# Kernel optimization log

Hardware: AMD Instinct MI355X
Metric: run time of the kernel (lower is better)

The kernel has to match this reference:

```python
import jax, jax.numpy as jnp
import numpy as np

# irreps config: (multiplicity, l) for "128x0e + 64x1o + 32x2e" (in == out)
IRREPS = [(128, 0), (64, 1), (32, 2)]


def setup_inputs() -> dict:
    key = jax.random.key(0)
    k0, k1, k2, k3 = jax.random.split(key, 4)
    N = 200000
    dim = sum(mul * (2 * l + 1) for mul, l in IRREPS)  # 480
    x = jax.random.normal(k0, (N, dim), dtype=jnp.float32)
    W0 = jax.random.normal(k1, (128, 128), dtype=jnp.float32)
    W1 = jax.random.normal(k2, (64, 64), dtype=jnp.float32)
    W2 = jax.random.normal(k3, (32, 32), dtype=jnp.float32)
    return {"x": x, "W0": W0, "W1": W1, "W2": W2}


def _irrep_linear(x, weights):
    # x: [N, dim_in]; per-irrep: reshape block to [N, mul, 2l+1], contract mul dim,
    # scale by 1/sqrt(fan_in) = 1/sqrt(mul_in) (e3nn default path normalization).
    outs = []
    off = 0
    for (mul, l), W in zip(IRREPS, weights):
        d = 2 * l + 1
        blk = x[:, off:off + mul * d].reshape(-1, mul, d)  # [N, mul, d]
        alpha = 1.0 / np.sqrt(mul)
        y = jnp.einsum('nid,io->nod', blk, W) * jnp.float32(alpha)  # [N, mul_out, d]
        outs.append(y.reshape(-1, mul * d))
        off += mul * d
    return jnp.concatenate(outs, axis=-1)  # [N, dim_out]


def reference(x, W0, W1, W2):
    return _irrep_linear(x, (W0, W1, W2))
```

## Files before the change

kernel.cpp:

```cpp
#include <hip/hip_runtime.h>

typedef _Float16 v8h __attribute__((ext_vector_type(8)));
typedef float    v4f __attribute__((ext_vector_type(4)));

#define MFMA16(a, b, c) __builtin_amdgcn_mfma_f32_16x16x32_f16((a), (b), (c), 0, 0, 0)

#define GLL16(gptr, lptr)                                                        \
  __builtin_amdgcn_global_load_lds((const __attribute__((address_space(1))) void*)(gptr), \
                                   (__attribute__((address_space(3))) void*)(lptr), 16, 0, 0)


__global__ void build_frags_k(const float* __restrict__ W0, const float* __restrict__ W1,
                              const float* __restrict__ W2, v8h* __restrict__ frag) {
  const int f = blockIdx.x;
  const int lane = threadIdx.x;
  int ot, kt;
  if (f < 32)       { ot = f >> 2;           kt = f & 3; }
  else if (f < 104) { int q = f - 32;  ot = 8 + q / 6;  kt = 4 + q % 6; }
  else              { int q = f - 104; ot = 20 + q / 5; kt = 10 + q % 5; }
  const int n  = ot * 16 + (lane & 15);
  const int kb = kt * 32 + (lane >> 4) * 8;
  v8h v;
#pragma unroll
  for (int e = 0; e < 8; ++e) {
    const int k = kb + e;
    float wv = 0.0f;
    if (k < 128) {
      if (n < 128) wv = W0[k * 128 + n] * 0.08838834764831845f;
    } else if (k < 320) {
      if (n >= 128 && n < 320) {
        const int i = k - 128, o = n - 128;
        if (i % 3 == o % 3) wv = W1[(i / 3) * 64 + (o / 3)] * 0.125f;
      }
    } else {
      if (n >= 320) {
        const int i = k - 320, o = n - 320;
        if (i % 5 == o % 5) wv = W2[(i / 5) * 32 + (o / 5)] * 0.17677669529663687f;
      }
    }
    v[e] = (_Float16)wv;
  }
  frag[f * 64 + lane] = v;
}

template <int V, int G>
__device__ __forceinline__ void wave_main(const float* __restrict__ x,
                                          const v8h* __restrict__ frag,
                                          float* __restrict__ out,
                                          unsigned char* sm, int t, int b, int nc) {
  const int lane = t & 63;
  const int w    = t >> 6;
  const int r16  = lane & 15;
  const int g    = lane >> 4;

  constexpr int S  = (V == 0) ? 4 : (V == 1) ? 3 : 5;
  constexpr int NF = (V == 0) ? 16 : (V == 1) ? 18 : 25;

  v8h f[NF];
  if constexpr (V == 0) {
#pragma unroll
    for (int i = 0; i < 4; ++i)
#pragma unroll
      for (int k = 0; k < 4; ++k)
        f[i * 4 + k] = frag[((w + 2 * i) * 4 + k) * 64 + lane];
  } else if constexpr (V == 1) {
#pragma unroll
    for (int i = 0; i < 3; ++i)
#pragma unroll
      for (int k = 0; k < 6; ++k)
        f[i * 6 + k] = frag[(32 + (w - 2 + 4 * i) * 6 + k) * 64 + lane];
  } else {
#pragma unroll
    for (int i = 0; i < 5; ++i)
#pragma unroll
      for (int k = 0; k < 5; ++k)
        f[i * 5 + k] = frag[(104 + (w - 6 + 2 * i) * 5 + k) * 64 + lane];
  }

  auto stage = [&](int tt, int slot) {
    const unsigned char* xt = (const unsigned char*)x + (size_t)tt * 30720u;
    unsigned char* buf = sm + (size_t)slot * 30720u;
#pragma unroll
    for (int i = 0; i < 4; ++i) {
      if (i < 3 || w < 6) {
        const unsigned gl = (unsigned)(i * 512 + t);
        const unsigned r  = gl / 120u;
        const unsigned j  = gl - r * 120u;
        GLL16(xt + r * 1920u + ((j ^ (r & 7u)) << 4), buf + i * 8192 + w * 1024);
      }
    }
  };

#define LDAF(kt, dst)                                                                       \
  {                                                                                         \
    const unsigned j0 = (unsigned)((kt) * 8 + g * 2);                                       \
    const float4 lo = *reinterpret_cast<const float4*>(smc + rb + (((j0) ^ q) << 4));       \
    const float4 hi = *reinterpret_cast<const float4*>(smc + rb + ((((j0) + 1) ^ q) << 4)); \
    v8h v_;                                                                                 \
    v_[0] = (_Float16)lo.x; v_[1] = (_Float16)lo.y;                                         \
    v_[2] = (_Float16)lo.z; v_[3] = (_Float16)lo.w;                                         \
    v_[4] = (_Float16)hi.x; v_[5] = (_Float16)hi.y;                                         \
    v_[6] = (_Float16)hi.z; v_[7] = (_Float16)hi.w;                                         \
    dst = v_;                                                                               \
  }

  auto compute = [&](int tt, int slot) {
    const unsigned char* smc = sm + (size_t)slot * 30720u;
    const unsigned rb = (unsigned)r16 * 1920u;
    const unsigned q  = (unsigned)(r16 & 7u);
    float* const ob = out + ((size_t)tt * 16 + r16) * 480 + g * 4;
    if constexpr (V == 0) {
      v8h xr[4];
#pragma unroll
      for (int k = 0; k < 4; ++k) LDAF(k, xr[k]);
#pragma unroll
      for (int i = 0; i < 4; ++i) {
        v4f a = {0.f, 0.f, 0.f, 0.f};
#pragma unroll
        for (int k = 0; k < 4; ++k) a = MFMA16(f[i * 4 + k], xr[k], a);
        *reinterpret_cast<v4f*>(ob + (w + 2 * i) * 16) = a;
      }
    } else if constexpr (V == 1) {
      v8h xr[6];
#pragma unroll
      for (int k = 0; k < 6; ++k) LDAF(4 + k, xr[k]);
#pragma unroll
      for (int i = 0; i < 3; ++i) {
        v4f a = {0.f, 0.f, 0.f, 0.f};
#pragma unroll
        for (int k = 0; k < 6; ++k) a = MFMA16(f[i * 6 + k], xr[k], a);
        *reinterpret_cast<v4f*>(ob + (6 + w + 4 * i) * 16) = a;
      }
    } else {
      v8h xr[5];
#pragma unroll
      for (int k = 0; k < 5; ++k) LDAF(10 + k, xr[k]);
#pragma unroll
      for (int i = 0; i < 5; ++i) {
        v4f a = {0.f, 0.f, 0.f, 0.f};
#pragma unroll
        for (int k = 0; k < 5; ++k) a = MFMA16(f[i * 5 + k], xr[k], a);
        *reinterpret_cast<v4f*>(ob + (14 + w + 2 * i) * 16) = a;
      }
    }
  };

#define PIPE(C, N)                                              \
  {                                                             \
    asm volatile("s_waitcnt vmcnt(%0)" :: "n"(N) : "memory");   \
    __builtin_amdgcn_s_barrier();                               \
    compute(b + (C) * 256, (C) & 3);                            \
  }

  stage(b, 0);
  stage(b + 256, 1);
  stage(b + 2 * 256, 2); PIPE(0, 2 * G)
  stage(b + 3 * 256, 3); PIPE(1, 2 * G + S)
  for (int c = 2; c <= nc - 3; ++c) {
    stage(b + (c + 2) * 256, (c + 2) & 3);
    PIPE(c, 2 * G + 2 * S)
  }
  PIPE(nc - 2, G + 2 * S)
  PIPE(nc - 1, 2 * S)
#undef PIPE
#undef LDAF
}

__global__ __launch_bounds__(512, 1) void irrep_linear_k(
    const float* __restrict__ x, const v8h* __restrict__ frag, float* __restrict__ out,
    int n_tiles) {
  __shared__ __align__(16) unsigned char sm[4 * 30720];
  const int t = threadIdx.x;
  const int b = blockIdx.x;
  const int nc = (n_tiles - b + 255) >> 8;
  const int w = t >> 6;
  if (w < 2)      wave_main<0, 4>(x, frag, out, sm, t, b, nc);
  else if (w < 6) wave_main<1, 4>(x, frag, out, sm, t, b, nc);
  else            wave_main<2, 3>(x, frag, out, sm, t, b, nc);
}

extern "C" void kernel_launch(void* const* d_in, const int* in_sizes, int n_in,
                              void* d_out, int out_size, void* d_ws, size_t ws_size,
                              hipStream_t stream) {
  const float* x  = (const float*)d_in[0];
  const float* W0 = (const float*)d_in[1];
  const float* W1 = (const float*)d_in[2];
  const float* W2 = (const float*)d_in[3];
  float* out = (float*)d_out;
  v8h* frag = (v8h*)d_ws;

  build_frags_k<<<154, 64, 0, stream>>>(W0, W1, W2, frag);

  const int N = in_sizes[0] / 480;
  const int n_tiles = N / 16;
  irrep_linear_k<<<256, 512, 0, stream>>>(x, frag, out, n_tiles);
}
```

Baseline: 150.0 us.

## Build weight fragments in-kernel and deepen LDS staging pipeline to five buffers

Removes the separate fragment-building kernel launch. Each wave now builds its f16 MFMA weight fragments directly from W0/W1/W2, after issuing the first three tile prefetches, so that work overlaps with the initial loads. The LDS ring grows from four to five 30 KB slots, keeping three tiles in flight instead of two, with vmcnt thresholds adjusted to match. The cost is redundant per-wave scattered weight loads and near-full LDS use. The compiler's wait on the weight loads may also serialise behind the first prefetches.

```diff
diff --git a/kernel.cpp b/kernel.cpp
--- a/kernel.cpp
+++ b/kernel.cpp
@@ -9,15 +9,10 @@
   __builtin_amdgcn_global_load_lds((const __attribute__((address_space(1))) void*)(gptr), \
                                    (__attribute__((address_space(3))) void*)(lptr), 16, 0, 0)
 
-
-__global__ void build_frags_k(const float* __restrict__ W0, const float* __restrict__ W1,
-                              const float* __restrict__ W2, v8h* __restrict__ frag) {
-  const int f = blockIdx.x;
-  const int lane = threadIdx.x;
-  int ot, kt;
-  if (f < 32)       { ot = f >> 2;           kt = f & 3; }
-  else if (f < 104) { int q = f - 32;  ot = 8 + q / 6;  kt = 4 + q % 6; }
-  else              { int q = f - 104; ot = 20 + q / 5; kt = 10 + q % 5; }
+__device__ __forceinline__ v8h build_frag(const float* __restrict__ W0,
+                                          const float* __restrict__ W1,
+                                          const float* __restrict__ W2,
+                                          int ot, int kt, int lane) {
   const int n  = ot * 16 + (lane & 15);
   const int kb = kt * 32 + (lane >> 4) * 8;
   v8h v;
@@ -40,12 +35,14 @@
     }
     v[e] = (_Float16)wv;
   }
-  frag[f * 64 + lane] = v;
+  return v;
 }
 
 template <int V, int G>
 __device__ __forceinline__ void wave_main(const float* __restrict__ x,
-                                          const v8h* __restrict__ frag,
+                                          const float* __restrict__ W0,
+                                          const float* __restrict__ W1,
+                                          const float* __restrict__ W2,
                                           float* __restrict__ out,
                                           unsigned char* sm, int t, int b, int nc) {
   const int lane = t & 63;
@@ -55,27 +52,6 @@
 
   constexpr int S  = (V == 0) ? 4 : (V == 1) ? 3 : 5;
   constexpr int NF = (V == 0) ? 16 : (V == 1) ? 18 : 25;
-
-  v8h f[NF];
-  if constexpr (V == 0) {
-#pragma unroll
-    for (int i = 0; i < 4; ++i)
-#pragma unroll
-      for (int k = 0; k < 4; ++k)
-        f[i * 4 + k] = frag[((w + 2 * i) * 4 + k) * 64 + lane];
-  } else if constexpr (V == 1) {
-#pragma unroll
-    for (int i = 0; i < 3; ++i)
-#pragma unroll
-      for (int k = 0; k < 6; ++k)
-        f[i * 6 + k] = frag[(32 + (w - 2 + 4 * i) * 6 + k) * 64 + lane];
-  } else {
-#pragma unroll
-    for (int i = 0; i < 5; ++i)
-#pragma unroll
-      for (int k = 0; k < 5; ++k)
-        f[i * 5 + k] = frag[(104 + (w - 6 + 2 * i) * 5 + k) * 64 + lane];
-  }
 
   auto stage = [&](int tt, int slot) {
     const unsigned char* xt = (const unsigned char*)x + (size_t)tt * 30720u;
@@ -90,6 +66,31 @@
       }
     }
   };
+
+  stage(b, 0);
+  stage(b + 256, 1);
+  stage(b + 2 * 256, 2);
+
+  v8h f[NF];
+  if constexpr (V == 0) {
+#pragma unroll
+    for (int i = 0; i < 4; ++i)
+#pragma unroll
+      for (int k = 0; k < 4; ++k)
+        f[i * 4 + k] = build_frag(W0, W1, W2, w + 2 * i, k, lane);
+  } else if constexpr (V == 1) {
+#pragma unroll
+    for (int i = 0; i < 3; ++i)
+#pragma unroll
+      for (int k = 0; k < 6; ++k)
+        f[i * 6 + k] = build_frag(W0, W1, W2, 6 + w + 4 * i, 4 + k, lane);
+  } else {
+#pragma unroll
+    for (int i = 0; i < 5; ++i)
+#pragma unroll
+      for (int k = 0; k < 5; ++k)
+        f[i * 5 + k] = build_frag(W0, W1, W2, 14 + w + 2 * i, 10 + k, lane);
+  }
 
 #define LDAF(kt, dst)                                                                       \
   {                                                                                         \
@@ -145,38 +146,42 @@
     }
   };
 
-#define PIPE(C, N)                                              \
+#define PIPE(C, SLOT, N)                                        \
   {                                                             \
     asm volatile("s_waitcnt vmcnt(%0)" :: "n"(N) : "memory");   \
     __builtin_amdgcn_s_barrier();                               \
-    compute(b + (C) * 256, (C) & 3);                            \
+    compute(b + (C) * 256, SLOT);                               \
   }
 
-  stage(b, 0);
-  stage(b + 256, 1);
-  stage(b + 2 * 256, 2); PIPE(0, 2 * G)
-  stage(b + 3 * 256, 3); PIPE(1, 2 * G + S)
-  for (int c = 2; c <= nc - 3; ++c) {
-    stage(b + (c + 2) * 256, (c + 2) & 3);
-    PIPE(c, 2 * G + 2 * S)
+  stage(b + 3 * 256, 3); PIPE(0, 0, 3 * G)
+  stage(b + 4 * 256, 4); PIPE(1, 1, 3 * G + S)
+  stage(b + 5 * 256, 0); PIPE(2, 2, 3 * G + 2 * S)
+  {
+    int ss = 1, sc = 3;
+    for (int c = 3; c <= nc - 4; ++c) {
+      stage(b + (c + 3) * 256, ss); ss = (ss == 4) ? 0 : ss + 1;
+      PIPE(c, sc, 3 * G + 3 * S)    sc = (sc == 4) ? 0 : sc + 1;
+    }
+    PIPE(nc - 3, sc, 2 * G + 3 * S) sc = (sc == 4) ? 0 : sc + 1;
+    PIPE(nc - 2, sc, G + 3 * S)     sc = (sc == 4) ? 0 : sc + 1;
+    PIPE(nc - 1, sc, 3 * S)
   }
-  PIPE(nc - 2, G + 2 * S)
-  PIPE(nc - 1, 2 * S)
 #undef PIPE
 #undef LDAF
 }
 
 __global__ __launch_bounds__(512, 1) void irrep_linear_k(
-    const float* __restrict__ x, const v8h* __restrict__ frag, float* __restrict__ out,
-    int n_tiles) {
-  __shared__ __align__(16) unsigned char sm[4 * 30720];
+    const float* __restrict__ x, const float* __restrict__ W0,
+    const float* __restrict__ W1, const float* __restrict__ W2,
+    float* __restrict__ out, int n_tiles) {
+  __shared__ __align__(16) unsigned char sm[5 * 30720];
   const int t = threadIdx.x;
   const int b = blockIdx.x;
   const int nc = (n_tiles - b + 255) >> 8;
   const int w = t >> 6;
-  if (w < 2)      wave_main<0, 4>(x, frag, out, sm, t, b, nc);
-  else if (w < 6) wave_main<1, 4>(x, frag, out, sm, t, b, nc);
-  else            wave_main<2, 3>(x, frag, out, sm, t, b, nc);
+  if (w < 2)      wave_main<0, 4>(x, W0, W1, W2, out, sm, t, b, nc);
+  else if (w < 6) wave_main<1, 4>(x, W0, W1, W2, out, sm, t, b, nc);
+  else            wave_main<2, 3>(x, W0, W1, W2, out, sm, t, b, nc);
 }
 
 extern "C" void kernel_launch(void* const* d_in, const int* in_sizes, int n_in,
@@ -187,11 +192,8 @@
   const float* W1 = (const float*)d_in[2];
   const float* W2 = (const float*)d_in[3];
   float* out = (float*)d_out;
-  v8h* frag = (v8h*)d_ws;
-
-  build_frags_k<<<154, 64, 0, stream>>>(W0, W1, W2, frag);
 
   const int N = in_sizes[0] / 480;
   const int n_tiles = N / 16;
-  irrep_linear_k<<<256, 512, 0, stream>>>(x, frag, out, n_tiles);
+  irrep_linear_k<<<256, 512, 0, stream>>>(x, W0, W1, W2, out, n_tiles);
 }
```

After: 192.9 us. +28.6%, slower.
